# Kernel optimization log

Measured on AMD Instinct MI355X. Metric: run time of the kernel, lower is better.

Reference implementation:

```python
import jax, jax.numpy as jnp
import numpy as np

H = 64          # index_n_heads
D = 128         # index_head_dim (== FP8 quant block size -> one scale per row)
RD = 64         # qk_rope_head_dim
TOPK = 512      # index_topk
THETA = 10000.0
SM_SCALE = D ** -0.5


def _fwht(x):
    """Sylvester-ordered fast Walsh-Hadamard transform over last dim, scaled by d^-0.5."""
    d = x.shape[-1]
    orig = x.shape
    y = x.reshape(-1, d)
    m = 1
    while m < d:  # static loop, log2(d)=7 iters
        y = y.reshape(-1, d // (2 * m), 2, m)
        a, b = y[:, :, 0, :], y[:, :, 1, :]
        y = jnp.stack([a + b, a - b], axis=2)
        m *= 2
    return y.reshape(orig) * (d ** -0.5)


def _interleaved_to_half(x):
    # [..., d] with (even, odd) interleaving -> [evens..., odds...]
    return jnp.concatenate([x[..., 0::2], x[..., 1::2]], axis=-1)


def _rope_half(x, cos, sin):
    # x: [..., RD] in half format; cos/sin broadcastable to [..., RD//2]
    x1, x2 = x[..., : RD // 2], x[..., RD // 2:]
    return jnp.concatenate([x1 * cos - x2 * sin, x2 * cos + x1 * sin], axis=-1)


def _layernorm(x, g, b, eps=1e-5):
    mu = jnp.mean(x, axis=-1, keepdims=True)
    var = jnp.mean(jnp.square(x - mu), axis=-1, keepdims=True)
    return (x - mu) * jax.lax.rsqrt(var + eps) * g + b


def _fp8_ue8m0_quant(x2d):
    """Per-row FP8 e4m3 quantization with UE8M0 (power-of-two) scales. x2d: (M, 128)."""
    amax = jnp.maximum(jnp.max(jnp.abs(x2d), axis=1), 1e-4)
    sf = jnp.exp2(jnp.ceil(jnp.log2(amax / 448.0)))               # (M,)
    xq = (x2d * (1.0 / sf)[:, None]).astype(jnp.float8_e4m3fn)
    return xq, sf


def _indexer_fwd(hidden_states, q_lora, positions, wq_b, wk, w_proj, ln_gamma, ln_beta):
    T = hidden_states.shape[0]
    # --- projections ---
    q = (q_lora @ wq_b).reshape(T, H, D)                          # (T,H,D)
    k = _layernorm(hidden_states @ wk, ln_gamma, ln_beta)         # (T,D)
    # --- RoPE on leading RD dims (interleaved -> half, then half rotation) ---
    inv_freq = 1.0 / (THETA ** (jnp.arange(0, RD, 2, dtype=jnp.float32) / RD))  # (RD/2,)
    ang = positions.astype(jnp.float32)[:, None] * inv_freq       # (T,RD/2)
    cos, sin = jnp.cos(ang), jnp.sin(ang)
    q_rot = _rope_half(_interleaved_to_half(q[..., :RD]), cos[:, None, :], sin[:, None, :])
    k_rot = _rope_half(_interleaved_to_half(k[..., :RD]), cos, sin)
    q = jnp.concatenate([q_rot, q[..., RD:]], axis=-1)
    k = jnp.concatenate([k_rot, k[..., RD:]], axis=-1)
    # --- Hadamard rotation ---
    q = _fwht(q)
    k = _fwht(k)
    # --- FP8 UE8M0 quantization (head_dim == quant block -> 1 scale per row) ---
    q_fp8, q_scale = _fp8_ue8m0_quant(q.reshape(T * H, D))
    k_fp8, k_scale = _fp8_ue8m0_quant(k)
    q_scale = q_scale.reshape(T, H)
    # --- gate weights: weights_proj * H^-0.5 * q_scale * softmax_scale ---
    weights = (hidden_states @ w_proj) * (H ** -0.5) * q_scale * SM_SCALE  # (T,H)
    # --- MQA indexer scoring: dequant matmul, ReLU, head-weighted sum ---
    qd = q_fp8.astype(jnp.float32).reshape(T, H, D)
    kd = k_fp8.astype(jnp.float32) * k_scale[:, None]             # (T,D)
    logits = jnp.einsum('thd,sd->ths', qd, kd)                    # (T,H,S)
    scores = jnp.einsum('th,ths->ts', weights, jax.nn.relu(logits))  # (T,S)
    # --- causal mask + top-k token selection ---
    t_idx = jnp.arange(T)
    causal = t_idx[None, :] <= t_idx[:, None]                     # (T,S): s <= t
    scores = jnp.where(causal, scores, jnp.float32(-1e30))
    vals, idx = jax.lax.top_k(scores, TOPK)
    return vals, idx


def setup_inputs() -> dict:
    key = jax.random.key(0)
    ks = jax.random.split(key, 5)
    T, HID, R = 1024, 7168, 1536
    return {
        'hidden_states': jax.random.normal(ks[0], (T, HID), jnp.float32),
        'q_lora': jax.random.normal(ks[1], (T, R), jnp.float32),
        'positions': jnp.arange(T, dtype=jnp.int32),
        'wq_b': jax.random.normal(ks[2], (R, H * D), jnp.float32) * (R ** -0.5),
        'wk': jax.random.normal(ks[3], (HID, D), jnp.float32) * (HID ** -0.5),
        'w_proj': jax.random.normal(ks[4], (HID, H), jnp.float32) * (HID ** -0.5),
        'ln_gamma': jnp.ones((D,), jnp.float32),
        'ln_beta': jnp.zeros((D,), jnp.float32),
    }


def reference(hidden_states, q_lora, positions, wq_b, wk, w_proj, ln_gamma, ln_beta):
    return _indexer_fwd(hidden_states, q_lora, positions, wq_b, wk, w_proj, ln_gamma, ln_beta)
```

## Files before the change

### kernel.cpp

```cpp
#include <hip/hip_runtime.h>
#include <cstdint>
#include <cmath>

#define NT 1024
#define NHID 7168
#define NR 1536
#define NH 64
#define ND 128
#define NTOPK 512
#define TTILE 4
#define KSPLIT 16

typedef float f32x4 __attribute__((ext_vector_type(4)));

__device__ __forceinline__ ushort f2bf(float x) {
  uint32_t u = __float_as_uint(x);
  u += 0x7fffu + ((u >> 16) & 1u);
  return (ushort)(u >> 16);
}
__device__ __forceinline__ float bf2f(ushort u) {
  return __uint_as_float(((uint32_t)u) << 16);
}
__device__ __forceinline__ void gload_lds16(const void* g, void* l) {
  __builtin_amdgcn_global_load_lds(
      (const __attribute__((address_space(1))) uint32_t*)g,
      (__attribute__((address_space(3))) uint32_t*)l, 16, 0, 0);
}
__device__ __forceinline__ uint32_t pk_fp8x4(float a, float b, float c, float d) {
  uint32_t lo = (uint32_t)__builtin_amdgcn_cvt_pk_fp8_f32(a, b, 0, false) & 0xffffu;
  uint32_t hi = (uint32_t)__builtin_amdgcn_cvt_pk_fp8_f32(c, d, 0, false) << 16;
  return lo | hi;
}

__device__ __forceinline__ void rope_fwht_quant(
    float v0, float v1, int l, int pos_t,
    const float* __restrict__ cost, const float* __restrict__ sint,
    uint8_t* __restrict__ out_bytes, float* __restrict__ out_scale) {
  float a = __shfl(v0, (2 * l) & 63, 64);
  float b = __shfl(v0, (2 * l + 1) & 63, 64);
  int fi = l & 31;
  float c = cost[pos_t * 32 + fi];
  float sn = sint[pos_t * 32 + fi];
  float r;
  if (l < 32)
    r = __fsub_rn(__fmul_rn(a, c), __fmul_rn(b, sn));
  else
    r = __fadd_rn(__fmul_rn(b, c), __fmul_rn(a, sn));
  v0 = r;

#pragma unroll
  for (int m = 1; m < 64; m <<= 1) {
    float p0 = __shfl_xor(v0, m, 64);
    float p1 = __shfl_xor(v1, m, 64);
    bool up = (l & m) == 0;
    v0 = up ? __fadd_rn(v0, p0) : __fsub_rn(p0, v0);
    v1 = up ? __fadd_rn(v1, p1) : __fsub_rn(p1, v1);
  }
  {
    float A0 = v0, B0 = v1;
    v0 = __fadd_rn(A0, B0);
    v1 = __fsub_rn(A0, B0);
  }
  const float WS = 0.08838834764831843f;
  v0 = __fmul_rn(v0, WS);
  v1 = __fmul_rn(v1, WS);

  float am = fmaxf(fabsf(v0), fabsf(v1));
#pragma unroll
  for (int m = 1; m < 64; m <<= 1) am = fmaxf(am, __shfl_xor(am, m, 64));
  am = fmaxf(am, 1e-4f);
  float ratio = __fdiv_rn(am, 448.0f);
  uint32_t rb = __float_as_uint(ratio);
  int e = (int)((rb + 0x7fffffu) >> 23) - 127;
  float sf = __uint_as_float((uint32_t)(e + 127) << 23);
  float inv = __uint_as_float((uint32_t)(127 - e) << 23);
  float q0 = __fmul_rn(v0, inv);
  float q1 = __fmul_rn(v1, inv);
  int b0 = __builtin_amdgcn_cvt_pk_fp8_f32(q0, q0, 0, false);
  int b1 = __builtin_amdgcn_cvt_pk_fp8_f32(q1, q1, 0, false);
  out_bytes[l] = (uint8_t)(b0 & 0xff);
  out_bytes[l + 64] = (uint8_t)(b1 & 0xff);
  if (l == 0) *out_scale = sf;
}

__global__ __launch_bounds__(256)
void prep_k(const float* __restrict__ hidden, const float* __restrict__ q_lora,
            const int* __restrict__ pos, uint32_t* __restrict__ hidden8,
            uint32_t* __restrict__ qlora8, float* __restrict__ cost,
            float* __restrict__ sint) {
  int gid = blockIdx.x * 256 + threadIdx.x;
  const int n8h = NT * NHID / 8;
  if (gid < n8h) {
    const f32x4* p = (const f32x4*)(hidden + (size_t)gid * 8);
    f32x4 a = p[0], b = p[1];
    hidden8[(size_t)gid * 2] = pk_fp8x4(a[0], a[1], a[2], a[3]);
    hidden8[(size_t)gid * 2 + 1] = pk_fp8x4(b[0], b[1], b[2], b[3]);
  } else {
    int i = gid - n8h;
    const f32x4* p = (const f32x4*)(q_lora + (size_t)i * 8);
    f32x4 a = p[0], b = p[1];
    qlora8[(size_t)i * 2] = pk_fp8x4(a[0], a[1], a[2], a[3]);
    qlora8[(size_t)i * 2 + 1] = pk_fp8x4(b[0], b[1], b[2], b[3]);
  }
  if (blockIdx.x < NT && threadIdx.x < 32) {
    int t = blockIdx.x, i = threadIdx.x;
    double x = (double)(2 * i) / 64.0;
    double pw = pow(10000.0, x);
    float p32 = (float)pw;
    float invf = __fdiv_rn(1.0f, p32);
    float ang = __fmul_rn((float)pos[t], invf);
    cost[t * 32 + i] = (float)cos((double)ang);
    sint[t * 32 + i] = (float)sin((double)ang);
  }
}

__global__ __launch_bounds__(256)
void tcast_kw_k(const float* __restrict__ wk, const float* __restrict__ wp,
                uint8_t* __restrict__ out) {
  __shared__ uint8_t t8[64][68];
  int tid = threadIdx.x;
  int bx = blockIdx.x;
  const float* in = (bx < 2) ? wk : wp;
  int N = (bx < 2) ? ND : NH;
  int n0 = (bx < 2) ? bx * 64 : 0;
  int orow0 = (bx < 2) ? bx * 64 : 128;
  int k0 = blockIdx.y * 64;
  int r = tid >> 4, c = (tid & 15) * 4;
#pragma unroll
  for (int rr = 0; rr < 64; rr += 16) {
    f32x4 v = *(const f32x4*)(in + (size_t)(k0 + rr + r) * N + n0 + c);
    *(uint32_t*)&t8[rr + r][c] =
        pk_fp8x4(v[0] * 64.0f, v[1] * 64.0f, v[2] * 64.0f, v[3] * 64.0f);
  }
  __syncthreads();
#pragma unroll
  for (int rr = 0; rr < 64; rr += 16) {
    int orow = rr + r;
    uint32_t w = (uint32_t)t8[c + 0][orow] | ((uint32_t)t8[c + 1][orow] << 8) |
                 ((uint32_t)t8[c + 2][orow] << 16) | ((uint32_t)t8[c + 3][orow] << 24);
    *(uint32_t*)(out + (size_t)(orow0 + orow) * NHID + k0 + c) = w;
  }
}

__global__ __launch_bounds__(256)
void tcast_fp8_k(const float* __restrict__ in, uint8_t* __restrict__ out,
                 int K, int N) {
  __shared__ uint8_t t8[64][68];
  int tid = threadIdx.x;
  int n0 = blockIdx.x * 64, k0 = blockIdx.y * 64;
  int r = tid >> 4, c = (tid & 15) * 4;
#pragma unroll
  for (int rr = 0; rr < 64; rr += 16) {
    f32x4 v = *(const f32x4*)(in + (size_t)(k0 + rr + r) * N + n0 + c);
    *(uint32_t*)&t8[rr + r][c] = pk_fp8x4(v[0], v[1], v[2], v[3]);
  }
  __syncthreads();
#pragma unroll
  for (int rr = 0; rr < 64; rr += 16) {
    int orow = rr + r;
    uint32_t w = (uint32_t)t8[c + 0][orow] | ((uint32_t)t8[c + 1][orow] << 8) |
                 ((uint32_t)t8[c + 2][orow] << 16) | ((uint32_t)t8[c + 3][orow] << 24);
    *(uint32_t*)(out + (size_t)(n0 + orow) * K + k0 + c) = w;
  }
}

__global__ __launch_bounds__(256)
void gemm_kw_k(const uint8_t* __restrict__ A, const uint8_t* __restrict__ Bt,
               float* __restrict__ C, int M, int N, int K, int kchunk) {
  __shared__ uint8_t As[2 * 64 * 64];
  __shared__ uint8_t Bs[2 * 64 * 64];
  int tid = threadIdx.x;
  int wave = tid >> 6, lane = tid & 63;
  int ln = lane & 15, lg = lane >> 4;
  int n0 = blockIdx.x * 64, m0 = blockIdx.y * 64;
  int k0 = blockIdx.z * kchunk;
  int wm = (wave >> 1) * 32, wn = (wave & 1) * 32;

  f32x4 acc[2][2];
#pragma unroll
  for (int m = 0; m < 2; m++)
#pragma unroll
    for (int n = 0; n < 2; n++) acc[m][n] = {0.f, 0.f, 0.f, 0.f};

  auto stage = [&](int buf, int kk0) {
    {
      int o = wave * 64 + lane;
      int row = o >> 2, g = o & 3;
      int gs = g ^ ((row >> 1) & 3);
      gload_lds16(A + (size_t)(m0 + row) * K + kk0 + gs * 16,
                  (char*)As + buf * 4096 + o * 16);
    }
    {
      int o = wave * 64 + lane;
      int row = o >> 2, g = o & 3;
      int gs = g ^ ((row >> 1) & 3);
      gload_lds16(Bt + (size_t)(n0 + row) * K + kk0 + gs * 16,
                  (char*)Bs + buf * 4096 + o * 16);
    }
  };

  int ntile = kchunk / 64;
  stage(0, k0);
  __syncthreads();
  int cur = 0;
  for (int t = 0; t < ntile; t++) {
    if (t + 1 < ntile) stage(cur ^ 1, k0 + (t + 1) * 64);
    const uint8_t* ap = As + cur * 4096;
    const uint8_t* bp = Bs + cur * 4096;
#pragma unroll
    for (int kk = 0; kk < 2; kk++) {
      long af[2], bfr[2];
#pragma unroll
      for (int m = 0; m < 2; m++) {
        int row = wm + m * 16 + ln;
        int g = kk * 2 + (lg >> 1);
        af[m] = *(const long*)(ap + row * 64 + ((g ^ ((row >> 1) & 3)) << 4) +
                               (lg & 1) * 8);
      }
#pragma unroll
      for (int n = 0; n < 2; n++) {
        int row = wn + n * 16 + ln;
        int g = kk * 2 + (lg >> 1);
        bfr[n] = *(const long*)(bp + row * 64 + ((g ^ ((row >> 1) & 3)) << 4) +
                                (lg & 1) * 8);
      }
#pragma unroll
      for (int m = 0; m < 2; m++)
#pragma unroll
        for (int n = 0; n < 2; n++)
          acc[m][n] = __builtin_amdgcn_mfma_f32_16x16x32_fp8_fp8(af[m], bfr[n],
                                                                 acc[m][n], 0, 0, 0);
    }
    __syncthreads();
    cur ^= 1;
  }

  float* Cz = C + (size_t)blockIdx.z * M * N;
#pragma unroll
  for (int m = 0; m < 2; m++)
#pragma unroll
    for (int n = 0; n < 2; n++)
#pragma unroll
      for (int j = 0; j < 4; j++) {
        int row = m0 + wm + m * 16 + lg * 4 + j;
        int col = n0 + wn + n * 16 + ln;
        Cz[(size_t)row * N + col] = acc[m][n][j];
      }
}

__global__ __launch_bounds__(256)
void gemm_q_fused_k(const uint8_t* __restrict__ A, const uint8_t* __restrict__ Bt,
                    const float* __restrict__ cost, const float* __restrict__ sint,
                    uint8_t* __restrict__ qfp8, float* __restrict__ qscale,
                    int M, int N, int K) {
  __shared__ char smem[24576];
  uint8_t* As = (uint8_t*)smem;
  uint8_t* Bs = (uint8_t*)smem + 8192;
  int tid = threadIdx.x;
  int wave = tid >> 6, lane = tid & 63;
  int ln = lane & 15, lg = lane >> 4;
  int n0 = blockIdx.x * 128, m0 = blockIdx.y * 64;
  int wm = (wave >> 1) * 32, wn = (wave & 1) * 64;

  f32x4 acc[2][4];
#pragma unroll
  for (int m = 0; m < 2; m++)
#pragma unroll
    for (int n = 0; n < 4; n++) acc[m][n] = {0.f, 0.f, 0.f, 0.f};

  auto stage = [&](int buf, int kk0) {
    {
      int o = wave * 64 + lane;
      int row = o >> 2, g = o & 3;
      int gs = g ^ ((row >> 1) & 3);
      gload_lds16(A + (size_t)(m0 + row) * K + kk0 + gs * 16,
                  (char*)As + buf * 4096 + o * 16);
    }
#pragma unroll
    for (int c = 0; c < 2; c++) {
      int o = c * 256 + wave * 64 + lane;
      int row = o >> 2, g = o & 3;
      int gs = g ^ ((row >> 1) & 3);
      gload_lds16(Bt + (size_t)(n0 + row) * K + kk0 + gs * 16,
                  (char*)Bs + buf * 8192 + o * 16);
    }
  };

  int ntile = K / 64;
  stage(0, 0);
  __syncthreads();
  int cur = 0;
  for (int t = 0; t < ntile; t++) {
    if (t + 1 < ntile) stage(cur ^ 1, (t + 1) * 64);
    const uint8_t* ap = As + cur * 4096;
    const uint8_t* bp = Bs + cur * 8192;
#pragma unroll
    for (int kk = 0; kk < 2; kk++) {
      long af[2], bfr[4];
#pragma unroll
      for (int m = 0; m < 2; m++) {
        int row = wm + m * 16 + ln;
        int g = kk * 2 + (lg >> 1);
        af[m] = *(const long*)(ap + row * 64 + ((g ^ ((row >> 1) & 3)) << 4) +
                               (lg & 1) * 8);
      }
#pragma unroll
      for (int n = 0; n < 4; n++) {
        int row = wn + n * 16 + ln;
        int g = kk * 2 + (lg >> 1);
        bfr[n] = *(const long*)(bp + row * 64 + ((g ^ ((row >> 1) & 3)) << 4) +
                                (lg & 1) * 8);
      }
#pragma unroll
      for (int m = 0; m < 2; m++)
#pragma unroll
        for (int n = 0; n < 4; n++)
          acc[m][n] = __builtin_amdgcn_mfma_f32_16x16x32_fp8_fp8(af[m], bfr[n],
                                                                 acc[m][n], 0, 0, 0);
    }
    __syncthreads();
    cur ^= 1;
  }

  ushort(*qtile)[132] = (ushort(*)[132])smem;
#pragma unroll
  for (int m = 0; m < 2; m++)
#pragma unroll
    for (int n = 0; n < 4; n++)
#pragma unroll
      for (int j = 0; j < 4; j++)
        qtile[wm + m * 16 + lg * 4 + j][wn + n * 16 + ln] = f2bf(acc[m][n][j]);
  __syncthreads();
  int h = blockIdx.x;
  for (int r = 0; r < 16; r++) {
    int row = wave * 16 + r;
    int tq = m0 + row;
    float v0 = bf2f(qtile[row][lane]);
    float v1 = bf2f(qtile[row][64 + lane]);
    rope_fwht_quant(v0, v1, lane, tq, cost, sint,
                    qfp8 + ((size_t)tq * NH + h) * ND,
                    qscale + (size_t)tq * NH + h);
  }
}

__global__ __launch_bounds__(256)
void kfin_weights_k(const float* __restrict__ kpart, const float* __restrict__ gamma,
                    const float* __restrict__ beta, const float* __restrict__ cost,
                    const float* __restrict__ sint, const float* __restrict__ qscale,
                    uint8_t* __restrict__ kfp8, float* __restrict__ kscale,
                    float* __restrict__ weights) {
  int l = threadIdx.x & 63;
  int row = blockIdx.x * 4 + (threadIdx.x >> 6);
  float v0 = 0.0f, v1 = 0.0f, ws = 0.0f;
#pragma unroll
  for (int p = 0; p < KSPLIT; p++) {
    const float* base = kpart + (size_t)p * (NT * 192) + row * 192;
    v0 = __fadd_rn(v0, base[l]);
    v1 = __fadd_rn(v1, base[l + 64]);
    ws = __fadd_rn(ws, base[128 + l]);
  }
  float w = __fmul_rn(ws, 0.001953125f);
  w = __fmul_rn(w, qscale[row * NH + l]);
  w = __fmul_rn(w, 0.08838834764831843f);
  weights[row * NH + l] = w;
  float s = __fadd_rn(v0, v1);
#pragma unroll
  for (int m = 1; m < 64; m <<= 1) s = __fadd_rn(s, __shfl_xor(s, m, 64));
  float mu = __fmul_rn(s, 0.0078125f);
  float d0 = __fsub_rn(v0, mu), d1 = __fsub_rn(v1, mu);
  float vs = __fadd_rn(__fmul_rn(d0, d0), __fmul_rn(d1, d1));
#pragma unroll
  for (int m = 1; m < 64; m <<= 1) vs = __fadd_rn(vs, __shfl_xor(vs, m, 64));
  float var = __fmul_rn(vs, 0.0078125f);
  float rs = (float)(1.0 / sqrt((double)__fadd_rn(var, 1e-5f)));
  v0 = __fadd_rn(__fmul_rn(__fmul_rn(d0, rs), gamma[l]), beta[l]);
  v1 = __fadd_rn(__fmul_rn(__fmul_rn(d1, rs), gamma[l + 64]), beta[l + 64]);
  rope_fwht_quant(v0, v1, l, row, cost, sint, kfp8 + (size_t)row * ND, kscale + row);
}

__global__ __launch_bounds__(256)
void scores_k(const uint8_t* __restrict__ qfp8, const uint8_t* __restrict__ kfp8,
              const float* __restrict__ weights, float* __restrict__ scores) {
  __shared__ uint8_t q_lds[TTILE * 64 * 128];
  __shared__ uint8_t k_lds[128 * 128];
  __shared__ float w_lds[TTILE * 64];

  int b = blockIdx.x;
  int g = 0;
  while (g < 7 && b >= 16 * (g + 1) * (g + 2)) g++;
  int r = b - 16 * g * (g + 1);
  int a = 32 * g + r / (g + 1);
  int chunk = r % (g + 1);
  int t0 = a * TTILE;
  int s0 = chunk * 128;

  int tid = threadIdx.x;
  int wave = tid >> 6, lane = tid & 63;
  int lg = lane >> 4, ln = lane & 15;

  const uint8_t* qbase = qfp8 + (size_t)t0 * 64 * 128;
#pragma unroll
  for (int it = 0; it < 8; it++) {
    int o = it * 256 + wave * 64 + lane;
    int row = o >> 3, G = o & 7;
    int src = row * 128 + ((G ^ ((row >> 1) & 7)) << 4);
    gload_lds16(qbase + src, q_lds + (it * 256 + wave * 64) * 16);
  }
  const uint8_t* kbase = kfp8 + (size_t)s0 * 128;
#pragma unroll
  for (int it = 0; it < 4; it++) {
    int o = it * 256 + wave * 64 + lane;
    int row = o >> 3, G = o & 7;
    int src = row * 128 + ((G ^ ((row >> 1) & 7)) << 4);
    gload_lds16(kbase + src, k_lds + (it * 256 + wave * 64) * 16);
  }
  w_lds[tid] = weights[t0 * NH + tid];
  __syncthreads();

  long bfr[2][4];
#pragma unroll
  for (int sj = 0; sj < 2; sj++) {
    int srow = wave * 32 + sj * 16 + ln;
    int base = srow * 128;
    int xr = ((srow >> 1) & 7) << 4;
#pragma unroll
    for (int ks = 0; ks < 4; ks++)
      bfr[sj][ks] = *(const long*)(k_lds + base + ((ks * 32 + lg * 8) ^ xr));
  }

  float p[TTILE][2];
#pragma unroll
  for (int tt = 0; tt < TTILE; tt++) p[tt][0] = p[tt][1] = 0.0f;

#pragma unroll
  for (int ht = 0; ht < 4; ht++) {
    long afr[TTILE][4];
#pragma unroll
    for (int tt = 0; tt < TTILE; tt++) {
      int qrow = tt * 64 + ht * 16 + ln;
      int base = qrow * 128;
      int xr = ((qrow >> 1) & 7) << 4;
#pragma unroll
      for (int ks = 0; ks < 4; ks++)
        afr[tt][ks] = *(const long*)(q_lds + base + ((ks * 32 + lg * 8) ^ xr));
    }
#pragma unroll
    for (int tt = 0; tt < TTILE; tt++) {
      float wj[4];
#pragma unroll
      for (int j = 0; j < 4; j++) wj[j] = w_lds[tt * 64 + ht * 16 + lg * 4 + j];
#pragma unroll
      for (int sj = 0; sj < 2; sj++) {
        f32x4 acc = {0.f, 0.f, 0.f, 0.f};
#pragma unroll
        for (int ks = 0; ks < 4; ks++)
          acc = __builtin_amdgcn_mfma_f32_16x16x32_fp8_fp8(afr[tt][ks], bfr[sj][ks],
                                                           acc, 0, 0, 0);
#pragma unroll
        for (int j = 0; j < 4; j++)
          p[tt][sj] = fmaf(wj[j], fmaxf(acc[j], 0.0f), p[tt][sj]);
      }
    }
  }

#pragma unroll
  for (int tt = 0; tt < TTILE; tt++)
#pragma unroll
    for (int sj = 0; sj < 2; sj++) {
      float v = p[tt][sj];
      v += __shfl_xor(v, 16, 64);
      v += __shfl_xor(v, 32, 64);
      if (lg == 0)
        scores[(size_t)(t0 + tt) * NT + s0 + wave * 32 + sj * 16 + ln] = v;
    }
}

__global__ __launch_bounds__(256)
void topk_k(const float* __restrict__ scores, const float* __restrict__ kscale,
            float* __restrict__ outv, float* __restrict__ outi) {
  __shared__ unsigned long long key[1024];
  int t = blockIdx.x, tid = threadIdx.x;
#pragma unroll
  for (int p = 0; p < 4; p++) {
    int s = tid + p * 256;
    float v;
    if (s <= t) {
      v = __fmul_rn(scores[(size_t)t * NT + s], kscale[s]);
    } else {
      v = -1e30f;
    }
    unsigned u = __float_as_uint(v);
    unsigned ou = (u & 0x80000000u) ? ~u : (u | 0x80000000u);
    key[s] = ((unsigned long long)ou << 32) | (unsigned)(~(unsigned)s);
  }
  for (int k = 2; k <= 1024; k <<= 1) {
    for (int j = k >> 1; j > 0; j >>= 1) {
      __syncthreads();
#pragma unroll
      for (int p = 0; p < 2; p++) {
        int i = tid + p * 256;
        int l = ((i & ~(j - 1)) << 1) | (i & (j - 1));
        int m = l + j;
        bool desc = ((l & k) == 0);
        unsigned long long a = key[l], b = key[m];
        if (desc ? (a < b) : (a > b)) {
          key[l] = b;
          key[m] = a;
        }
      }
    }
  }
  __syncthreads();
#pragma unroll
  for (int p = 0; p < 2; p++) {
    int r = tid + p * 256;
    unsigned long long kk = key[r];
    unsigned ou = (unsigned)(kk >> 32);
    unsigned u = (ou & 0x80000000u) ? (ou ^ 0x80000000u) : ~ou;
    unsigned idx = (~(unsigned)(kk & 0xffffffffu)) & 1023u;
    outv[(size_t)t * NTOPK + r] = __uint_as_float(u);
    outi[(size_t)t * NTOPK + r] = (float)idx;
  }
}

extern "C" void kernel_launch(void* const* d_in, const int* in_sizes, int n_in,
                              void* d_out, int out_size, void* d_ws, size_t ws_size,
                              hipStream_t stream) {
  const float* hidden = (const float*)d_in[0];
  const float* q_lora = (const float*)d_in[1];
  const int* positions = (const int*)d_in[2];
  const float* wq_b = (const float*)d_in[3];
  const float* wk = (const float*)d_in[4];
  const float* w_proj = (const float*)d_in[5];
  const float* ln_g = (const float*)d_in[6];
  const float* ln_b = (const float*)d_in[7];
  float* out = (float*)d_out;

  char* u0 = (char*)d_ws;
  uint8_t* hidden8 = (uint8_t*)u0;
  uint8_t* wkp8 = (uint8_t*)(u0 + 7340032);
  uint8_t* wqb8 = (uint8_t*)u0;
  uint8_t* qlora8 = (uint8_t*)(u0 + 12582912);
  float* scores = (float*)u0;
  char* p = u0 + 14680064;
  float* kpart = (float*)p;    p += 12582912;
  float* cost = (float*)p;     p += 131072;
  float* sint = (float*)p;     p += 131072;
  float* kscale = (float*)p;   p += 4096;
  float* qscale = (float*)p;   p += 262144;
  float* weights = (float*)p;  p += 262144;
  uint8_t* kfp8 = (uint8_t*)p; p += 131072;
  uint8_t* qfp8 = (uint8_t*)p; p += 8388608;

  prep_k<<<(NT * NHID / 8 + NT * NR / 8) / 256, 256, 0, stream>>>(
      hidden, q_lora, positions, (uint32_t*)hidden8, (uint32_t*)qlora8,
      cost, sint);

  tcast_kw_k<<<dim3(3, 112), 256, 0, stream>>>(wk, w_proj, wkp8);
  gemm_kw_k<<<dim3(3, 16, KSPLIT), 256, 0, stream>>>(
      hidden8, wkp8, kpart, NT, 192, NHID, NHID / KSPLIT);

  tcast_fp8_k<<<dim3(128, 24), 256, 0, stream>>>(wq_b, wqb8, NR, NH * ND);
  gemm_q_fused_k<<<dim3(64, 16), 256, 0, stream>>>(
      qlora8, wqb8, cost, sint, qfp8, qscale, NT, NH * ND, NR);

  kfin_weights_k<<<NT / 4, 256, 0, stream>>>(kpart, ln_g, ln_b, cost, sint,
                                             qscale, kfp8, kscale, weights);

  scores_k<<<1152, 256, 0, stream>>>(qfp8, kfp8, weights, scores);
  topk_k<<<NT, 256, 0, stream>>>(scores, kscale, out, out + (size_t)NT * NTOPK);
}
```

Before: 119.9 us.

## Unify FP8 GEMMs into templated kernel with deeper prefetch and larger tiles

Replaces the two FP8 MFMA GEMM kernels with one templated kernel. It issues two stages ahead and uses explicit vmcnt waits with raw barriers instead of __syncthreads, so global-to-LDS loads overlap compute better. It also enlarges the block tiles to 128x64 for the K/weights GEMM and 128x128 for the Q GEMM, halving the block count and raising per-wave MFMA work and reuse. The risks are the hand-tuned vmcnt counts, which must match the number of outstanding loads, and possible occupancy loss from larger LDS and register use.

```diff
diff --git a/kernel.cpp b/kernel.cpp
--- a/kernel.cpp
+++ b/kernel.cpp
@@ -164,182 +164,129 @@
   }
 }
 
-__global__ __launch_bounds__(256)
-void gemm_kw_k(const uint8_t* __restrict__ A, const uint8_t* __restrict__ Bt,
-               float* __restrict__ C, int M, int N, int K, int kchunk) {
-  __shared__ uint8_t As[2 * 64 * 64];
-  __shared__ uint8_t Bs[2 * 64 * 64];
+template <int BM, int BN, bool FUSEQ>
+__global__ __launch_bounds__(256)
+void gemm_fp8_pipe_k(const uint8_t* __restrict__ A, const uint8_t* __restrict__ Bt,
+                     float* __restrict__ C, const float* __restrict__ cost,
+                     const float* __restrict__ sint, uint8_t* __restrict__ qfp8,
+                     float* __restrict__ qscale, int M, int N, int K, int kchunk) {
+  constexpr int FM = BM / 32;
+  constexpr int FN = BN / 32;
+  constexpr int ABYTES = BM * 64;
+  constexpr int BBYTES = BN * 64;
+  constexpr int BUF = ABYTES + BBYTES;
+  constexpr int LPS = (BM + BN) / 64;
+  constexpr int SMEM = FUSEQ ? (128 * 132 * 2) : 2 * BUF;
+  __shared__ char smem[SMEM];
   int tid = threadIdx.x;
   int wave = tid >> 6, lane = tid & 63;
   int ln = lane & 15, lg = lane >> 4;
-  int n0 = blockIdx.x * 64, m0 = blockIdx.y * 64;
+  int n0 = blockIdx.x * BN, m0 = blockIdx.y * BM;
   int k0 = blockIdx.z * kchunk;
-  int wm = (wave >> 1) * 32, wn = (wave & 1) * 32;
-
-  f32x4 acc[2][2];
-#pragma unroll
-  for (int m = 0; m < 2; m++)
-#pragma unroll
-    for (int n = 0; n < 2; n++) acc[m][n] = {0.f, 0.f, 0.f, 0.f};
+  int wm = (wave >> 1) * (BM / 2), wn = (wave & 1) * (BN / 2);
+
+  f32x4 acc[FM][FN];
+#pragma unroll
+  for (int m = 0; m < FM; m++)
+#pragma unroll
+    for (int n = 0; n < FN; n++) acc[m][n] = {0.f, 0.f, 0.f, 0.f};
 
   auto stage = [&](int buf, int kk0) {
-    {
-      int o = wave * 64 + lane;
+    char* base = smem + buf * BUF;
+#pragma unroll
+    for (int c = 0; c < BM / 64; c++) {
+      int o = c * 256 + wave * 64 + lane;
       int row = o >> 2, g = o & 3;
       int gs = g ^ ((row >> 1) & 3);
-      gload_lds16(A + (size_t)(m0 + row) * K + kk0 + gs * 16,
-                  (char*)As + buf * 4096 + o * 16);
-    }
-    {
-      int o = wave * 64 + lane;
+      gload_lds16(A + (size_t)(m0 + row) * K + kk0 + gs * 16, base + o * 16);
+    }
+#pragma unroll
+    for (int c = 0; c < BN / 64; c++) {
+      int o = c * 256 + wave * 64 + lane;
       int row = o >> 2, g = o & 3;
       int gs = g ^ ((row >> 1) & 3);
       gload_lds16(Bt + (size_t)(n0 + row) * K + kk0 + gs * 16,
-                  (char*)Bs + buf * 4096 + o * 16);
+                  base + ABYTES + o * 16);
     }
   };
 
   int ntile = kchunk / 64;
   stage(0, k0);
-  __syncthreads();
+  stage(1, k0 + 64);
   int cur = 0;
   for (int t = 0; t < ntile; t++) {
-    if (t + 1 < ntile) stage(cur ^ 1, k0 + (t + 1) * 64);
-    const uint8_t* ap = As + cur * 4096;
-    const uint8_t* bp = Bs + cur * 4096;
+    if (t < ntile - 1) {
+      if constexpr (LPS == 4)
+        asm volatile("s_waitcnt vmcnt(4)" ::: "memory");
+      else
+        asm volatile("s_waitcnt vmcnt(3)" ::: "memory");
+    } else {
+      asm volatile("s_waitcnt vmcnt(0)" ::: "memory");
+    }
+    __builtin_amdgcn_s_barrier();
+    const uint8_t* ap = (const uint8_t*)smem + cur * BUF;
+    const uint8_t* bp = ap + ABYTES;
 #pragma unroll
     for (int kk = 0; kk < 2; kk++) {
-      long af[2], bfr[2];
-#pragma unroll
-      for (int m = 0; m < 2; m++) {
+      long af[FM], bf[FN];
+#pragma unroll
+      for (int m = 0; m < FM; m++) {
         int row = wm + m * 16 + ln;
         int g = kk * 2 + (lg >> 1);
         af[m] = *(const long*)(ap + row * 64 + ((g ^ ((row >> 1) & 3)) << 4) +
                                (lg & 1) * 8);
       }
 #pragma unroll
-      for (int n = 0; n < 2; n++) {
+      for (int n = 0; n < FN; n++) {
         int row = wn + n * 16 + ln;
         int g = kk * 2 + (lg >> 1);
-        bfr[n] = *(const long*)(bp + row * 64 + ((g ^ ((row >> 1) & 3)) << 4) +
-                                (lg & 1) * 8);
-      }
-#pragma unroll
-      for (int m = 0; m < 2; m++)
-#pragma unroll
-        for (int n = 0; n < 2; n++)
-          acc[m][n] = __builtin_amdgcn_mfma_f32_16x16x32_fp8_fp8(af[m], bfr[n],
-                                                                 acc[m][n], 0, 0, 0);
-    }
-    __syncthreads();
-    cur ^= 1;
-  }
-
-  float* Cz = C + (size_t)blockIdx.z * M * N;
-#pragma unroll
-  for (int m = 0; m < 2; m++)
-#pragma unroll
-    for (int n = 0; n < 2; n++)
-#pragma unroll
-      for (int j = 0; j < 4; j++) {
-        int row = m0 + wm + m * 16 + lg * 4 + j;
-        int col = n0 + wn + n * 16 + ln;
-        Cz[(size_t)row * N + col] = acc[m][n][j];
-      }
-}
-
-__global__ __launch_bounds__(256)
-void gemm_q_fused_k(const uint8_t* __restrict__ A, const uint8_t* __restrict__ Bt,
-                    const float* __restrict__ cost, const float* __restrict__ sint,
-                    uint8_t* __restrict__ qfp8, float* __restrict__ qscale,
-                    int M, int N, int K) {
-  __shared__ char smem[24576];
-  uint8_t* As = (uint8_t*)smem;
-  uint8_t* Bs = (uint8_t*)smem + 8192;
-  int tid = threadIdx.x;
-  int wave = tid >> 6, lane = tid & 63;
-  int ln = lane & 15, lg = lane >> 4;
-  int n0 = blockIdx.x * 128, m0 = blockIdx.y * 64;
-  int wm = (wave >> 1) * 32, wn = (wave & 1) * 64;
-
-  f32x4 acc[2][4];
-#pragma unroll
-  for (int m = 0; m < 2; m++)
-#pragma unroll
-    for (int n = 0; n < 4; n++) acc[m][n] = {0.f, 0.f, 0.f, 0.f};
-
-  auto stage = [&](int buf, int kk0) {
-    {
-      int o = wave * 64 + lane;
-      int row = o >> 2, g = o & 3;
-      int gs = g ^ ((row >> 1) & 3);
-      gload_lds16(A + (size_t)(m0 + row) * K + kk0 + gs * 16,
-                  (char*)As + buf * 4096 + o * 16);
-    }
-#pragma unroll
-    for (int c = 0; c < 2; c++) {
-      int o = c * 256 + wave * 64 + lane;
-      int row = o >> 2, g = o & 3;
-      int gs = g ^ ((row >> 1) & 3);
-      gload_lds16(Bt + (size_t)(n0 + row) * K + kk0 + gs * 16,
-                  (char*)Bs + buf * 8192 + o * 16);
-    }
-  };
-
-  int ntile = K / 64;
-  stage(0, 0);
-  __syncthreads();
-  int cur = 0;
-  for (int t = 0; t < ntile; t++) {
-    if (t + 1 < ntile) stage(cur ^ 1, (t + 1) * 64);
-    const uint8_t* ap = As + cur * 4096;
-    const uint8_t* bp = Bs + cur * 8192;
-#pragma unroll
-    for (int kk = 0; kk < 2; kk++) {
-      long af[2], bfr[4];
-#pragma unroll
-      for (int m = 0; m < 2; m++) {
-        int row = wm + m * 16 + ln;
-        int g = kk * 2 + (lg >> 1);
-        af[m] = *(const long*)(ap + row * 64 + ((g ^ ((row >> 1) & 3)) << 4) +
+        bf[n] = *(const long*)(bp + row * 64 + ((g ^ ((row >> 1) & 3)) << 4) +
                                (lg & 1) * 8);
       }
 #pragma unroll
-      for (int n = 0; n < 4; n++) {
-        int row = wn + n * 16 + ln;
-        int g = kk * 2 + (lg >> 1);
-        bfr[n] = *(const long*)(bp + row * 64 + ((g ^ ((row >> 1) & 3)) << 4) +
-                                (lg & 1) * 8);
-      }
-#pragma unroll
-      for (int m = 0; m < 2; m++)
-#pragma unroll
-        for (int n = 0; n < 4; n++)
-          acc[m][n] = __builtin_amdgcn_mfma_f32_16x16x32_fp8_fp8(af[m], bfr[n],
+      for (int m = 0; m < FM; m++)
+#pragma unroll
+        for (int n = 0; n < FN; n++)
+          acc[m][n] = __builtin_amdgcn_mfma_f32_16x16x32_fp8_fp8(af[m], bf[n],
                                                                  acc[m][n], 0, 0, 0);
     }
+    __builtin_amdgcn_s_barrier();
+    if (t + 2 < ntile) stage(cur, k0 + (t + 2) * 64);
+    cur ^= 1;
+  }
+
+  if constexpr (FUSEQ) {
+    ushort(*qtile)[132] = (ushort(*)[132])smem;
+#pragma unroll
+    for (int m = 0; m < FM; m++)
+#pragma unroll
+      for (int n = 0; n < FN; n++)
+#pragma unroll
+        for (int j = 0; j < 4; j++)
+          qtile[wm + m * 16 + lg * 4 + j][wn + n * 16 + ln] = f2bf(acc[m][n][j]);
     __syncthreads();
-    cur ^= 1;
-  }
-
-  ushort(*qtile)[132] = (ushort(*)[132])smem;
-#pragma unroll
-  for (int m = 0; m < 2; m++)
-#pragma unroll
-    for (int n = 0; n < 4; n++)
-#pragma unroll
-      for (int j = 0; j < 4; j++)
-        qtile[wm + m * 16 + lg * 4 + j][wn + n * 16 + ln] = f2bf(acc[m][n][j]);
-  __syncthreads();
-  int h = blockIdx.x;
-  for (int r = 0; r < 16; r++) {
-    int row = wave * 16 + r;
-    int tq = m0 + row;
-    float v0 = bf2f(qtile[row][lane]);
-    float v1 = bf2f(qtile[row][64 + lane]);
-    rope_fwht_quant(v0, v1, lane, tq, cost, sint,
-                    qfp8 + ((size_t)tq * NH + h) * ND,
-                    qscale + (size_t)tq * NH + h);
+    int h = blockIdx.x;
+    for (int r = 0; r < 32; r++) {
+      int row = wave * 32 + r;
+      int tq = m0 + row;
+      float v0 = bf2f(qtile[row][lane]);
+      float v1 = bf2f(qtile[row][64 + lane]);
+      rope_fwht_quant(v0, v1, lane, tq, cost, sint,
+                      qfp8 + ((size_t)tq * NH + h) * ND,
+                      qscale + (size_t)tq * NH + h);
+    }
+  } else {
+    float* Cz = C + (size_t)blockIdx.z * M * N;
+#pragma unroll
+    for (int m = 0; m < FM; m++)
+#pragma unroll
+      for (int n = 0; n < FN; n++)
+#pragma unroll
+        for (int j = 0; j < 4; j++) {
+          int row = m0 + wm + m * 16 + lg * 4 + j;
+          int col = n0 + wn + n * 16 + ln;
+          Cz[(size_t)row * N + col] = acc[m][n][j];
+        }
   }
 }
 
@@ -557,12 +504,14 @@
       cost, sint);
 
   tcast_kw_k<<<dim3(3, 112), 256, 0, stream>>>(wk, w_proj, wkp8);
-  gemm_kw_k<<<dim3(3, 16, KSPLIT), 256, 0, stream>>>(
-      hidden8, wkp8, kpart, NT, 192, NHID, NHID / KSPLIT);
+  gemm_fp8_pipe_k<128, 64, false><<<dim3(3, 8, KSPLIT), 256, 0, stream>>>(
+      hidden8, wkp8, kpart, nullptr, nullptr, nullptr, nullptr,
+      NT, 192, NHID, NHID / KSPLIT);
 
   tcast_fp8_k<<<dim3(128, 24), 256, 0, stream>>>(wq_b, wqb8, NR, NH * ND);
-  gemm_q_fused_k<<<dim3(64, 16), 256, 0, stream>>>(
-      qlora8, wqb8, cost, sint, qfp8, qscale, NT, NH * ND, NR);
+  gemm_fp8_pipe_k<128, 128, true><<<dim3(64, 8, 1), 256, 0, stream>>>(
+      qlora8, wqb8, nullptr, cost, sint, qfp8, qscale,
+      NT, NH * ND, NR, NR);
 
   kfin_weights_k<<<NT / 4, 256, 0, stream>>>(kpart, ln_g, ln_b, cost, sint,
                                              qscale, kfp8, kscale, weights);
```

Measured after the change: 128.5 us. 1.07x slower.
